# Kernel optimization log

Hardware: AMD Instinct MI355X
Metric: run time of the kernel (lower is better)

Reference implementation:

```python
import jax, jax.numpy as jnp
import numpy as np

N = 50000   # nodes
E = 800000  # edges (avg degree 16)
D = 96      # feature dim for all layers


def setup_inputs() -> dict:
    key = jax.random.key(0)
    ks = jax.random.split(key, 8)
    x = jax.random.normal(ks[0], (N, D), dtype=jnp.float32)
    edge_index = jax.random.randint(ks[1], (2, E), 0, N, dtype=jnp.int32)
    edge_weight = jax.random.uniform(ks[2], (E,), dtype=jnp.float32)
    batch = jnp.zeros((N,), dtype=jnp.int32)  # unused by forward, kept for signature fidelity
    s = 1.0 / np.sqrt(D)
    W1 = jax.random.normal(ks[3], (D, D), dtype=jnp.float32) * s
    b1 = jnp.zeros((D,), dtype=jnp.float32)
    W2 = jax.random.normal(ks[4], (D, D), dtype=jnp.float32) * s
    b2 = jnp.zeros((D,), dtype=jnp.float32)
    return {"x": x, "edge_index": edge_index, "edge_weight": edge_weight,
            "batch": batch, "W1": W1, "b1": b1, "W2": W2, "b2": b2}


def gcn_conv(x, row, col, ew, W, b):
    """PyG GCNConv: add self-loops (weight 1), symmetric normalization,
    linear transform then weighted scatter-add aggregation at target (col)."""
    n = x.shape[0]
    h = x @ W  # [N, D_out]
    # degree includes self-loop weight 1.0
    deg = jax.ops.segment_sum(ew, col, num_segments=n) + 1.0
    dinv = jnp.where(deg > 0, jax.lax.rsqrt(deg), 0.0)
    norm = dinv[row] * ew * dinv[col]                      # [E]
    agg = jax.ops.segment_sum(h[row] * norm[:, None], col, num_segments=n)
    agg = agg + h * (dinv * dinv)[:, None]                 # self-loop messages
    return agg + b


def reference(x, edge_index, edge_weight, batch, W1, b1, W2, b2):
    row, col = edge_index[0], edge_index[1]
    # layer 1: conv -> relu (dropout p=0.0 is a no-op)
    h = jax.nn.relu(gcn_conv(x, row, col, edge_weight, W1, b1))
    # layer 2
    h = jax.nn.relu(gcn_conv(h, row, col, edge_weight, W2, b2))
    return h
```

## Files before the change

kernel.cpp:

```cpp
#include <hip/hip_runtime.h>
#include <hip/hip_fp16.h>

#define DIM 96
#define DIM4 (DIM/4)

typedef _Float16 f16x8 __attribute__((ext_vector_type(8)));
typedef float    f32x4 __attribute__((ext_vector_type(4)));

#define WSCALE 4194304.0f


#define PREP_BLOCKS 256

__global__ __launch_bounds__(256) void prep_kernel(unsigned long long* __restrict__ pdeg,
                                                   const float* __restrict__ W1,
                                                   const float* __restrict__ W2,
                                                   _Float16* __restrict__ Bt1,
                                                   _Float16* __restrict__ Bt2, int n) {
    for (int i = blockIdx.x * 256 + threadIdx.x; i < n; i += PREP_BLOCKS * 256)
        pdeg[i] = 0ULL;
    int i = blockIdx.x * 256 + threadIdx.x;
    if (i < DIM * DIM) {
        int c = i / DIM, k = i - c * DIM;
        Bt1[i] = (_Float16)W1[k * DIM + c];
        Bt2[i] = (_Float16)W2[k * DIM + c];
    }
}


__global__ void edge_pack_kernel(const int* __restrict__ col, const float* __restrict__ ew,
                                 unsigned long long* __restrict__ pdeg,
                                 int* __restrict__ rank, int e) {
    int i = blockIdx.x * blockDim.x + threadIdx.x;
    if (i < e) {
        unsigned q = (unsigned)(ew[i] * WSCALE + 0.5f);
        unsigned long long old =
            atomicAdd(&pdeg[col[i]], (1ULL << 32) | (unsigned long long)q);
        rank[i] = (int)(old >> 32);
    }
}


#define SCAN_BLK 256
#define SCAN_ELEMS 1024

__global__ __launch_bounds__(SCAN_BLK) void dinv_scanA_kernel(const unsigned long long* __restrict__ pdeg,
                                                              float* __restrict__ dinv,
                                                              int* __restrict__ cnt,
                                                              int* __restrict__ bsum, int n) {
    __shared__ int sdata[SCAN_BLK];
    int base = blockIdx.x * SCAN_ELEMS;
    int s = 0;
#pragma unroll
    for (int j = 0; j < 4; ++j) {
        int i = base + j * SCAN_BLK + (int)threadIdx.x;
        if (i < n) {
            unsigned long long p = pdeg[i];
            int c = (int)(p >> 32);
            cnt[i] = c;
            s += c;
            float deg = 1.0f + (float)(p & 0xffffffffULL) * (1.0f / WSCALE);
            dinv[i] = rsqrtf(deg);
        }
    }
    sdata[threadIdx.x] = s;
    __syncthreads();
    for (int off = SCAN_BLK / 2; off > 0; off >>= 1) {
        if (threadIdx.x < (unsigned)off) sdata[threadIdx.x] += sdata[threadIdx.x + off];
        __syncthreads();
    }
    if (threadIdx.x == 0) bsum[blockIdx.x] = sdata[0];
}

__global__ __launch_bounds__(1024) void scan_phaseB(int* __restrict__ bsum,
                                                    int* __restrict__ rowptr, int nb, int n) {
    __shared__ int sdata[1024];
    int v = (threadIdx.x < (unsigned)nb) ? bsum[threadIdx.x] : 0;
    sdata[threadIdx.x] = v;
    __syncthreads();
    for (int off = 1; off < 1024; off <<= 1) {
        int t = (threadIdx.x >= (unsigned)off) ? sdata[threadIdx.x - off] : 0;
        __syncthreads();
        sdata[threadIdx.x] += t;
        __syncthreads();
    }
    if (threadIdx.x < (unsigned)nb) bsum[threadIdx.x] = sdata[threadIdx.x] - v;
    if (threadIdx.x == (unsigned)(nb - 1)) rowptr[n] = sdata[threadIdx.x];
}

__global__ __launch_bounds__(SCAN_BLK) void scan_phaseC(const int* __restrict__ cnt,
                                                        const int* __restrict__ bsum,
                                                        int* __restrict__ rowptr, int n) {
    __shared__ int sdata[SCAN_BLK];
    int base = blockIdx.x * SCAN_ELEMS + (int)threadIdx.x * 4;
    int v[4];
#pragma unroll
    for (int j = 0; j < 4; ++j) v[j] = (base + j < n) ? cnt[base + j] : 0;
    int tsum = v[0] + v[1] + v[2] + v[3];
    sdata[threadIdx.x] = tsum;
    __syncthreads();
    for (int off = 1; off < SCAN_BLK; off <<= 1) {
        int t = (threadIdx.x >= (unsigned)off) ? sdata[threadIdx.x - off] : 0;
        __syncthreads();
        sdata[threadIdx.x] += t;
        __syncthreads();
    }
    int excl = bsum[blockIdx.x] + sdata[threadIdx.x] - tsum;
#pragma unroll
    for (int j = 0; j < 4; ++j) {
        if (base + j < n) rowptr[base + j] = excl;
        excl += v[j];
    }
}


__global__ void fill_kernel(const int* __restrict__ row, const int* __restrict__ col,
                            const float* __restrict__ ew, const float* __restrict__ dinv,
                            const int* __restrict__ rowptr, const int* __restrict__ rank,
                            int2* __restrict__ spack, int e) {
    int i = blockIdx.x * blockDim.x + threadIdx.x;
    if (i < e) {
        int c = col[i];
        int r = row[i];
        int p = rowptr[c] + rank[i];
        spack[p] = make_int2(r, __float_as_int(ew[i] * dinv[r]));
    }
}


template<bool A_IS_F32>
__global__ __launch_bounds__(256) void gemm_mfma_kernel(const void* __restrict__ Av,
                                                        const _Float16* __restrict__ Bt,
                                                        _Float16* __restrict__ H, int n) {
    int wave = threadIdx.x >> 6;
    int lane = threadIdx.x & 63;
    int r0 = blockIdx.x * 64 + wave * 16;
    if (r0 >= n) return;

    int lrow = lane & 15;
    int lk   = (lane >> 4) << 3;
    int arow = r0 + lrow;
    if (arow > n - 1) arow = n - 1;

    const _Float16* Ah = (const _Float16*)Av;
    const float*    Af = (const float*)Av;

    f32x4 acc[6] = {};

#pragma unroll
    for (int ks = 0; ks < 3; ++ks) {
        int k0 = ks * 32 + lk;
        f16x8 a;
        if (A_IS_F32) {
            const float* ap = Af + (size_t)arow * DIM + k0;
            float4 x0 = *(const float4*)ap;
            float4 x1 = *(const float4*)(ap + 4);
            a[0] = (_Float16)x0.x; a[1] = (_Float16)x0.y;
            a[2] = (_Float16)x0.z; a[3] = (_Float16)x0.w;
            a[4] = (_Float16)x1.x; a[5] = (_Float16)x1.y;
            a[6] = (_Float16)x1.z; a[7] = (_Float16)x1.w;
        } else {
            a = *(const f16x8*)(Ah + (size_t)arow * DIM + k0);
        }
#pragma unroll
        for (int ct = 0; ct < 6; ++ct) {
            f16x8 b = *(const f16x8*)(Bt + (size_t)(ct * 16 + lrow) * DIM + k0);
            acc[ct] = __builtin_amdgcn_mfma_f32_16x16x32_f16(a, b, acc[ct], 0, 0, 0);
        }
    }

    int crow = r0 + ((lane >> 4) << 2);
    int ccol = lane & 15;
#pragma unroll
    for (int ct = 0; ct < 6; ++ct) {
#pragma unroll
        for (int j = 0; j < 4; ++j) {
            int rr = crow + j;
            if (rr < n) H[(size_t)rr * DIM + ct * 16 + ccol] = (_Float16)acc[ct][j];
        }
    }
}


#define GLN 12
#define GNPB 16

__device__ __forceinline__ float4 half4_to_float4_u2(unsigned a, unsigned b) {
    __half2 h01 = *(const __half2*)&a;
    __half2 h23 = *(const __half2*)&b;
    float2 f01 = __half22float2(h01);
    float2 f23 = __half22float2(h23);
    return make_float4(f01.x, f01.y, f23.x, f23.y);
}

template<bool OUT_F32>
__global__ __launch_bounds__(192) void gather_kernel(const int* __restrict__ rowptr,
                                                     const int2* __restrict__ spack,
                                                     const float* __restrict__ dinv,
                                                     const __half* __restrict__ H,
                                                     const float* __restrict__ bias,
                                                     float* __restrict__ outf,
                                                     __half* __restrict__ outh, int n) {
    int ln = threadIdx.x / GLN;
    int q  = threadIdx.x - ln * GLN;
    int node = blockIdx.x * GNPB + ln;
    if (node >= n) return;

    int beg = rowptr[node];
    int end = rowptr[node + 1];
    float di = dinv[node];

    const uint4* Hq = (const uint4*)H;

    float4 accA = make_float4(0.f, 0.f, 0.f, 0.f);
    float4 accB = make_float4(0.f, 0.f, 0.f, 0.f);
    int p = beg;
    for (; p + 3 < end; p += 4) {
        int2 e0 = spack[p];
        int2 e1 = spack[p + 1];
        int2 e2 = spack[p + 2];
        int2 e3 = spack[p + 3];
        uint4 v0 = Hq[e0.x * 12 + q];
        uint4 v1 = Hq[e1.x * 12 + q];
        uint4 v2 = Hq[e2.x * 12 + q];
        uint4 v3 = Hq[e3.x * 12 + q];
        float w0 = __int_as_float(e0.y);
        float w1 = __int_as_float(e1.y);
        float w2 = __int_as_float(e2.y);
        float w3 = __int_as_float(e3.y);
        float4 a0 = half4_to_float4_u2(v0.x, v0.y), b0 = half4_to_float4_u2(v0.z, v0.w);
        float4 a1 = half4_to_float4_u2(v1.x, v1.y), b1 = half4_to_float4_u2(v1.z, v1.w);
        float4 a2 = half4_to_float4_u2(v2.x, v2.y), b2 = half4_to_float4_u2(v2.z, v2.w);
        float4 a3 = half4_to_float4_u2(v3.x, v3.y), b3 = half4_to_float4_u2(v3.z, v3.w);
        accA.x = fmaf(w0, a0.x, accA.x); accA.y = fmaf(w0, a0.y, accA.y);
        accA.z = fmaf(w0, a0.z, accA.z); accA.w = fmaf(w0, a0.w, accA.w);
        accB.x = fmaf(w0, b0.x, accB.x); accB.y = fmaf(w0, b0.y, accB.y);
        accB.z = fmaf(w0, b0.z, accB.z); accB.w = fmaf(w0, b0.w, accB.w);
        accA.x = fmaf(w1, a1.x, accA.x); accA.y = fmaf(w1, a1.y, accA.y);
        accA.z = fmaf(w1, a1.z, accA.z); accA.w = fmaf(w1, a1.w, accA.w);
        accB.x = fmaf(w1, b1.x, accB.x); accB.y = fmaf(w1, b1.y, accB.y);
        accB.z = fmaf(w1, b1.z, accB.z); accB.w = fmaf(w1, b1.w, accB.w);
        accA.x = fmaf(w2, a2.x, accA.x); accA.y = fmaf(w2, a2.y, accA.y);
        accA.z = fmaf(w2, a2.z, accA.z); accA.w = fmaf(w2, a2.w, accA.w);
        accB.x = fmaf(w2, b2.x, accB.x); accB.y = fmaf(w2, b2.y, accB.y);
        accB.z = fmaf(w2, b2.z, accB.z); accB.w = fmaf(w2, b2.w, accB.w);
        accA.x = fmaf(w3, a3.x, accA.x); accA.y = fmaf(w3, a3.y, accA.y);
        accA.z = fmaf(w3, a3.z, accA.z); accA.w = fmaf(w3, a3.w, accA.w);
        accB.x = fmaf(w3, b3.x, accB.x); accB.y = fmaf(w3, b3.y, accB.y);
        accB.z = fmaf(w3, b3.z, accB.z); accB.w = fmaf(w3, b3.w, accB.w);
    }
    for (; p < end; ++p) {
        int2 e0 = spack[p];
        float w0 = __int_as_float(e0.y);
        uint4 v0 = Hq[e0.x * 12 + q];
        float4 a0 = half4_to_float4_u2(v0.x, v0.y), b0 = half4_to_float4_u2(v0.z, v0.w);
        accA.x = fmaf(w0, a0.x, accA.x); accA.y = fmaf(w0, a0.y, accA.y);
        accA.z = fmaf(w0, a0.z, accA.z); accA.w = fmaf(w0, a0.w, accA.w);
        accB.x = fmaf(w0, b0.x, accB.x); accB.y = fmaf(w0, b0.y, accB.y);
        accB.z = fmaf(w0, b0.z, accB.z); accB.w = fmaf(w0, b0.w, accB.w);
    }

    float s = di * di;
    uint4 hv = Hq[node * 12 + q];
    float4 hcA = half4_to_float4_u2(hv.x, hv.y);
    float4 hcB = half4_to_float4_u2(hv.z, hv.w);
    float4 bA = ((const float4*)bias)[2 * q];
    float4 bB = ((const float4*)bias)[2 * q + 1];

    float4 oA, oB;
    oA.x = fmaxf(fmaf(hcA.x, s, accA.x * di) + bA.x, 0.0f);
    oA.y = fmaxf(fmaf(hcA.y, s, accA.y * di) + bA.y, 0.0f);
    oA.z = fmaxf(fmaf(hcA.z, s, accA.z * di) + bA.z, 0.0f);
    oA.w = fmaxf(fmaf(hcA.w, s, accA.w * di) + bA.w, 0.0f);
    oB.x = fmaxf(fmaf(hcB.x, s, accB.x * di) + bB.x, 0.0f);
    oB.y = fmaxf(fmaf(hcB.y, s, accB.y * di) + bB.y, 0.0f);
    oB.z = fmaxf(fmaf(hcB.z, s, accB.z * di) + bB.z, 0.0f);
    oB.w = fmaxf(fmaf(hcB.w, s, accB.w * di) + bB.w, 0.0f);

    if (OUT_F32) {
        ((float4*)(outf + (size_t)node * DIM))[2 * q]     = oA;
        ((float4*)(outf + (size_t)node * DIM))[2 * q + 1] = oB;
    } else {
        __half2 p01 = __float22half2_rn(make_float2(oA.x, oA.y));
        __half2 p23 = __float22half2_rn(make_float2(oA.z, oA.w));
        __half2 p45 = __float22half2_rn(make_float2(oB.x, oB.y));
        __half2 p67 = __float22half2_rn(make_float2(oB.z, oB.w));
        uint4 u;
        u.x = *(const unsigned*)&p01;
        u.y = *(const unsigned*)&p23;
        u.z = *(const unsigned*)&p45;
        u.w = *(const unsigned*)&p67;
        ((uint4*)outh)[node * 12 + q] = u;
    }
}


extern "C" void kernel_launch(void* const* d_in, const int* in_sizes, int n_in,
                              void* d_out, int out_size, void* d_ws, size_t ws_size,
                              hipStream_t stream) {
    const float* x   = (const float*)d_in[0];
    const int*   ei  = (const int*)d_in[1];
    const float* ew  = (const float*)d_in[2];
    const float* W1  = (const float*)d_in[4];
    const float* b1  = (const float*)d_in[5];
    const float* W2  = (const float*)d_in[6];
    const float* b2  = (const float*)d_in[7];

    const int N = in_sizes[0] / DIM;
    const int E = in_sizes[1] / 2;
    const int* row = ei;
    const int* col = ei + E;

    const int NB = (N + SCAN_ELEMS - 1) / SCAN_ELEMS;

    char* ws = (char*)d_ws;
    size_t off = 0;
    auto alloc = [&](size_t bytes) { void* p = ws + off; off = (off + bytes + 255) & ~(size_t)255; return p; };
    unsigned long long* pdeg = (unsigned long long*)alloc((size_t)N * 8);
    float* dinv   = (float*)alloc((size_t)N * 4);
    int*   cnt    = (int*)  alloc((size_t)N * 4);
    int*   rowptr = (int*)  alloc((size_t)(N + 1) * 4);
    int*   bsum   = (int*)  alloc((size_t)NB * 4);
    int*   rank   = (int*)  alloc((size_t)E * 4);
    int2*  spack  = (int2*) alloc((size_t)E * 8);
    _Float16* A   = (_Float16*)alloc((size_t)N * DIM * 2);
    _Float16* y1h = (_Float16*)alloc((size_t)N * DIM * 2);
    _Float16* Bt1 = (_Float16*)alloc((size_t)DIM * DIM * 2);
    _Float16* Bt2 = (_Float16*)alloc((size_t)DIM * DIM * 2);
    float* out    = (float*)d_out;

    dim3 blk(256);
    int gE  = (E + 255) / 256;
    int gMM = (N + 63) / 64;
    int gG  = (N + GNPB - 1) / GNPB;

    prep_kernel<<<PREP_BLOCKS, blk, 0, stream>>>(pdeg, W1, W2, Bt1, Bt2, N);
    edge_pack_kernel<<<gE, blk, 0, stream>>>(col, ew, pdeg, rank, E);
    dinv_scanA_kernel<<<NB, SCAN_BLK, 0, stream>>>(pdeg, dinv, cnt, bsum, N);
    scan_phaseB<<<1, 1024, 0, stream>>>(bsum, rowptr, NB, N);
    scan_phaseC<<<NB, SCAN_BLK, 0, stream>>>(cnt, bsum, rowptr, N);
    fill_kernel<<<gE, blk, 0, stream>>>(row, col, ew, dinv, rowptr, rank, spack, E);

    gemm_mfma_kernel<true><<<gMM, blk, 0, stream>>>(x, Bt1, A, N);
    gather_kernel<false><<<gG, 192, 0, stream>>>(rowptr, spack, dinv, (const __half*)A, b1,
                                                 nullptr, (__half*)y1h, N);

    gemm_mfma_kernel<false><<<gMM, blk, 0, stream>>>(y1h, Bt2, A, N);
    gather_kernel<true><<<gG, 192, 0, stream>>>(rowptr, spack, dinv, (const __half*)A, b2,
                                                out, nullptr, N);
}
```

Before: 153.6 us.

## Compress CSR edge entries to 32-bit and fold block-sum scan into phase C

Packs each CSR entry as a 16-bit source node index plus an fp16 normalized weight in one 32-bit word, and stores per-edge rank as 16-bit. It also removes the separate single-block scan kernel by having every phase-C block redo the small block-sum scan in shared memory. This halves edge-metadata traffic in fill and both gathers and drops a launch. In exchange it assumes fewer than 65536 nodes, per-node degree and at most 64 scan blocks, and lowers edge weight precision to fp16.

```diff
diff --git a/kernel.cpp b/kernel.cpp
--- a/kernel.cpp
+++ b/kernel.cpp
@@ -30,13 +30,13 @@
 
 __global__ void edge_pack_kernel(const int* __restrict__ col, const float* __restrict__ ew,
                                  unsigned long long* __restrict__ pdeg,
-                                 int* __restrict__ rank, int e) {
+                                 unsigned short* __restrict__ rank, int e) {
     int i = blockIdx.x * blockDim.x + threadIdx.x;
     if (i < e) {
         unsigned q = (unsigned)(ew[i] * WSCALE + 0.5f);
         unsigned long long old =
             atomicAdd(&pdeg[col[i]], (1ULL << 32) | (unsigned long long)q);
-        rank[i] = (int)(old >> 32);
+        rank[i] = (unsigned short)(old >> 32);
     }
 }
 
@@ -72,26 +72,24 @@
     if (threadIdx.x == 0) bsum[blockIdx.x] = sdata[0];
 }
 
-__global__ __launch_bounds__(1024) void scan_phaseB(int* __restrict__ bsum,
-                                                    int* __restrict__ rowptr, int nb, int n) {
-    __shared__ int sdata[1024];
-    int v = (threadIdx.x < (unsigned)nb) ? bsum[threadIdx.x] : 0;
-    sdata[threadIdx.x] = v;
-    __syncthreads();
-    for (int off = 1; off < 1024; off <<= 1) {
-        int t = (threadIdx.x >= (unsigned)off) ? sdata[threadIdx.x - off] : 0;
-        __syncthreads();
-        sdata[threadIdx.x] += t;
-        __syncthreads();
-    }
-    if (threadIdx.x < (unsigned)nb) bsum[threadIdx.x] = sdata[threadIdx.x] - v;
-    if (threadIdx.x == (unsigned)(nb - 1)) rowptr[n] = sdata[threadIdx.x];
-}
 
 __global__ __launch_bounds__(SCAN_BLK) void scan_phaseC(const int* __restrict__ cnt,
                                                         const int* __restrict__ bsum,
-                                                        int* __restrict__ rowptr, int n) {
+                                                        int* __restrict__ rowptr, int n, int nb) {
     __shared__ int sdata[SCAN_BLK];
+    __shared__ int sb[64];
+    if (threadIdx.x < 64)
+        sb[threadIdx.x] = ((int)threadIdx.x < nb) ? bsum[threadIdx.x] : 0;
+    __syncthreads();
+    for (int off = 1; off < 64; off <<= 1) {
+        int t = (threadIdx.x < 64 && threadIdx.x >= (unsigned)off) ? sb[threadIdx.x - off] : 0;
+        __syncthreads();
+        if (threadIdx.x < 64) sb[threadIdx.x] += t;
+        __syncthreads();
+    }
+    int blockbase = (blockIdx.x == 0) ? 0 : sb[blockIdx.x - 1];
+    if (blockIdx.x == 0 && threadIdx.x == 0) rowptr[n] = sb[nb - 1];
+
     int base = blockIdx.x * SCAN_ELEMS + (int)threadIdx.x * 4;
     int v[4];
 #pragma unroll
@@ -105,7 +103,7 @@
         sdata[threadIdx.x] += t;
         __syncthreads();
     }
-    int excl = bsum[blockIdx.x] + sdata[threadIdx.x] - tsum;
+    int excl = blockbase + sdata[threadIdx.x] - tsum;
 #pragma unroll
     for (int j = 0; j < 4; ++j) {
         if (base + j < n) rowptr[base + j] = excl;
@@ -116,14 +114,16 @@
 
 __global__ void fill_kernel(const int* __restrict__ row, const int* __restrict__ col,
                             const float* __restrict__ ew, const float* __restrict__ dinv,
-                            const int* __restrict__ rowptr, const int* __restrict__ rank,
-                            int2* __restrict__ spack, int e) {
+                            const int* __restrict__ rowptr, const unsigned short* __restrict__ rank,
+                            unsigned* __restrict__ spack, int e) {
     int i = blockIdx.x * blockDim.x + threadIdx.x;
     if (i < e) {
         int c = col[i];
         int r = row[i];
-        int p = rowptr[c] + rank[i];
-        spack[p] = make_int2(r, __float_as_int(ew[i] * dinv[r]));
+        int p = rowptr[c] + (int)rank[i];
+        float w = ew[i] * dinv[r];
+        unsigned hb = (unsigned)__half_as_ushort(__float2half_rn(w));
+        spack[p] = ((unsigned)r << 16) | hb;
     }
 }
 
@@ -193,9 +193,13 @@
     return make_float4(f01.x, f01.y, f23.x, f23.y);
 }
 
+__device__ __forceinline__ float wdec(unsigned e) {
+    return __half2float(__ushort_as_half((unsigned short)(e & 0xffffu)));
+}
+
 template<bool OUT_F32>
 __global__ __launch_bounds__(192) void gather_kernel(const int* __restrict__ rowptr,
-                                                     const int2* __restrict__ spack,
+                                                     const unsigned* __restrict__ spack,
                                                      const float* __restrict__ dinv,
                                                      const __half* __restrict__ H,
                                                      const float* __restrict__ bias,
@@ -216,18 +220,15 @@
     float4 accB = make_float4(0.f, 0.f, 0.f, 0.f);
     int p = beg;
     for (; p + 3 < end; p += 4) {
-        int2 e0 = spack[p];
-        int2 e1 = spack[p + 1];
-        int2 e2 = spack[p + 2];
-        int2 e3 = spack[p + 3];
-        uint4 v0 = Hq[e0.x * 12 + q];
-        uint4 v1 = Hq[e1.x * 12 + q];
-        uint4 v2 = Hq[e2.x * 12 + q];
-        uint4 v3 = Hq[e3.x * 12 + q];
-        float w0 = __int_as_float(e0.y);
-        float w1 = __int_as_float(e1.y);
-        float w2 = __int_as_float(e2.y);
-        float w3 = __int_as_float(e3.y);
+        unsigned e0 = spack[p];
+        unsigned e1 = spack[p + 1];
+        unsigned e2 = spack[p + 2];
+        unsigned e3 = spack[p + 3];
+        uint4 v0 = Hq[(e0 >> 16) * 12 + q];
+        uint4 v1 = Hq[(e1 >> 16) * 12 + q];
+        uint4 v2 = Hq[(e2 >> 16) * 12 + q];
+        uint4 v3 = Hq[(e3 >> 16) * 12 + q];
+        float w0 = wdec(e0), w1 = wdec(e1), w2 = wdec(e2), w3 = wdec(e3);
         float4 a0 = half4_to_float4_u2(v0.x, v0.y), b0 = half4_to_float4_u2(v0.z, v0.w);
         float4 a1 = half4_to_float4_u2(v1.x, v1.y), b1 = half4_to_float4_u2(v1.z, v1.w);
         float4 a2 = half4_to_float4_u2(v2.x, v2.y), b2 = half4_to_float4_u2(v2.z, v2.w);
@@ -250,9 +251,9 @@
         accB.z = fmaf(w3, b3.z, accB.z); accB.w = fmaf(w3, b3.w, accB.w);
     }
     for (; p < end; ++p) {
-        int2 e0 = spack[p];
-        float w0 = __int_as_float(e0.y);
-        uint4 v0 = Hq[e0.x * 12 + q];
+        unsigned e0 = spack[p];
+        float w0 = wdec(e0);
+        uint4 v0 = Hq[(e0 >> 16) * 12 + q];
         float4 a0 = half4_to_float4_u2(v0.x, v0.y), b0 = half4_to_float4_u2(v0.z, v0.w);
         accA.x = fmaf(w0, a0.x, accA.x); accA.y = fmaf(w0, a0.y, accA.y);
         accA.z = fmaf(w0, a0.z, accA.z); accA.w = fmaf(w0, a0.w, accA.w);
@@ -321,8 +322,8 @@
     int*   cnt    = (int*)  alloc((size_t)N * 4);
     int*   rowptr = (int*)  alloc((size_t)(N + 1) * 4);
     int*   bsum   = (int*)  alloc((size_t)NB * 4);
-    int*   rank   = (int*)  alloc((size_t)E * 4);
-    int2*  spack  = (int2*) alloc((size_t)E * 8);
+    unsigned short* rank = (unsigned short*)alloc((size_t)E * 2);
+    unsigned* spack = (unsigned*)alloc((size_t)E * 4);
     _Float16* A   = (_Float16*)alloc((size_t)N * DIM * 2);
     _Float16* y1h = (_Float16*)alloc((size_t)N * DIM * 2);
     _Float16* Bt1 = (_Float16*)alloc((size_t)DIM * DIM * 2);
@@ -337,8 +338,7 @@
     prep_kernel<<<PREP_BLOCKS, blk, 0, stream>>>(pdeg, W1, W2, Bt1, Bt2, N);
     edge_pack_kernel<<<gE, blk, 0, stream>>>(col, ew, pdeg, rank, E);
     dinv_scanA_kernel<<<NB, SCAN_BLK, 0, stream>>>(pdeg, dinv, cnt, bsum, N);
-    scan_phaseB<<<1, 1024, 0, stream>>>(bsum, rowptr, NB, N);
-    scan_phaseC<<<NB, SCAN_BLK, 0, stream>>>(cnt, bsum, rowptr, N);
+    scan_phaseC<<<NB, SCAN_BLK, 0, stream>>>(cnt, bsum, rowptr, N, NB);
     fill_kernel<<<gE, blk, 0, stream>>>(row, col, ew, dinv, rowptr, rank, spack, E);
 
     gemm_mfma_kernel<true><<<gMM, blk, 0, stream>>>(x, Bt1, A, N);
```

Result: faster. 148.3 us (-3.5%).
